# Kernel tuning notes

Measured on AMD Instinct MI355X. Metric: run time of the kernel, lower is better.

The kernel has to match this reference:

```python
import jax, jax.numpy as jnp
import numpy as np

B, D, E, K, HID, RH, NL, EMB = 4096, 1024, 8, 2, 512, 256, 24, 32


def _ln(y, g, b, eps=1e-5):
    mu = y.mean(-1, keepdims=True)
    var = y.var(-1, keepdims=True)
    return (y - mu) / jnp.sqrt(var + eps) * g + b


def setup_inputs() -> dict:
    key = jax.random.key(0)
    ks = jax.random.split(key, 16)
    s = 0.02
    return {
        "h": jax.random.normal(ks[0], (B, D), jnp.float32),
        "x": jax.random.normal(ks[1], (B, D), jnp.float32),
        "layer_idx": 5,
        "layer_emb": jax.random.normal(ks[2], (NL, EMB)) * s,
        "phase_emb": jax.random.normal(ks[3], (2, EMB)) * s,
        "Wr1": jax.random.normal(ks[4], (2 * D + 2 * EMB, RH)) * s,
        "br1": jnp.zeros((RH,)),
        "lnr_g": jnp.ones((RH,)),
        "lnr_b": jnp.zeros((RH,)),
        "Wr2": jax.random.normal(ks[5], (RH, E)) * s,
        "br2": jnp.zeros((E,)),
        "W1": jax.random.normal(ks[6], (E, 2 * D, HID)) * s,
        "b1": jnp.zeros((E, HID)),
        "ln1_g": jnp.ones((E, HID)),
        "ln1_b": jnp.zeros((E, HID)),
        "W2": jax.random.normal(ks[7], (E, HID, 4 * D)) * s,
        "b2": jnp.zeros((E, 4 * D)),
        "Wa": jax.random.normal(ks[8], (E, D, D)) * s,
        "ba": jnp.zeros((E, D)),
        "Wb": jax.random.normal(ks[9], (E, D, D)) * s,
        "bb": jnp.zeros((E, D)),
        "Wg": jax.random.normal(ks[10], (E, D, D)) * s,
        "bg": jnp.zeros((E, D)),
        "Wv": jax.random.normal(ks[11], (E, D, D)) * s,
        "bv": jnp.zeros((E, D)),
    }


def reference(h, x, layer_idx, layer_emb, phase_emb, Wr1, br1, lnr_g, lnr_b,
              Wr2, br2, W1, b1, ln1_g, ln1_b, W2, b2,
              Wa, ba, Wb, bb, Wg, bg, Wv, bv):
    Bn = h.shape[0]
    # --- router ---
    le = jnp.broadcast_to(layer_emb[layer_idx], (Bn, EMB))
    pe = jnp.broadcast_to(phase_emb[0], (Bn, EMB))  # phase='equilibrium' -> idx 0
    ri = jnp.concatenate([h, x, le, pe], axis=-1)   # [B, 2D+64]
    rhid = jax.nn.gelu(_ln(ri @ Wr1 + br1, lnr_g, lnr_b), approximate=False)
    logits = rhid @ Wr2 + br2                       # [B, E]
    top_vals, top_idx = jax.lax.top_k(logits, K)    # [B, K]
    w = jax.nn.softmax(top_vals, axis=-1)           # [B, K]
    # --- all experts (vectorized over E), then gather top-k per token ---
    hx = jnp.concatenate([h, x], axis=-1)           # [B, 2D]
    hid = jnp.einsum('bi,eio->ebo', hx, W1) + b1[:, None]          # [E, B, HID]
    hid = jax.nn.gelu(_ln(hid, ln1_g[:, None], ln1_b[:, None]), approximate=False)
    feats = jnp.einsum('ebh,eho->ebo', hid, W2) + b2[:, None]      # [E, B, 4D]
    af, bf, gf, vf = jnp.split(feats, 4, axis=-1)
    alpha = jax.nn.sigmoid(jnp.einsum('ebd,edo->ebo', af, Wa) + ba[:, None])
    beta = jax.nn.softplus(jnp.einsum('ebd,edo->ebo', bf, Wb) + bb[:, None])
    gate = jax.nn.sigmoid(jnp.einsum('ebd,edo->ebo', gf, Wg) + bg[:, None])
    vcd = jnp.einsum('ebd,edo->ebo', vf, Wv) + bv[:, None]
    allo = jnp.stack([alpha, beta, gate, vcd])       # [4, E, B, D]
    sel = allo[:, top_idx, jnp.arange(Bn)[:, None]]  # [4, B, K, D]
    out = jnp.einsum('bk,obkd->obd', w, sel)         # [4, B, D]
    return out
```

## Files before the change

kernel.cpp:

```cpp
#include <hip/hip_runtime.h>
#include <hip/hip_bf16.h>

#define B_TOK   4096
#define D_DIM   1024
#define E_NUM   8
#define HID_DIM 512
#define RH_DIM  256
#define EMB_DIM 32
#define NPAIR   (B_TOK * 2)
#define CPAD    32

typedef __attribute__((ext_vector_type(8))) short    bf16x8;
typedef __attribute__((ext_vector_type(8))) unsigned short u16x8;
typedef __attribute__((ext_vector_type(4))) unsigned short u16x4;
typedef __attribute__((ext_vector_type(4))) float    f32x4;

__device__ __forceinline__ unsigned short f2bf(float f) {
    union { float f; unsigned u; } v; v.f = f;
    unsigned r = (v.u + 0x7fffu + ((v.u >> 16) & 1u)) >> 16;
    return (unsigned short)r;
}
__device__ __forceinline__ float bf2f(unsigned short b) {
    union { unsigned u; float f; } v; v.u = ((unsigned)b) << 16;
    return v.f;
}

__device__ __forceinline__ void glds16(const void* g, void* l) {
    __builtin_amdgcn_global_load_lds(
        (const __attribute__((address_space(1))) unsigned int*)g,
        (__attribute__((address_space(3))) unsigned int*)l, 16, 0, 0);
}

__device__ inline float apply_act(float v, int a) {
    if (a == 0 || a == 2) return 1.f / (1.f + __expf(-v));
    if (a == 1) return fmaxf(v, 0.f) + __logf(1.f + __expf(-fabsf(v)));
    return v;
}

__global__ void k_hxbf(const float* __restrict__ h, const float* __restrict__ x,
                       unsigned short* __restrict__ hi, unsigned short* __restrict__ lo) {
    int gid = blockIdx.x * 256 + threadIdx.x;
    int token = gid >> 8;
    int c0 = (gid & 255) * 8;
    const float* src = (c0 < 1024) ? (h + (size_t)token * 1024 + c0)
                                   : (x + (size_t)token * 1024 + c0 - 1024);
    u16x8 oh, ol;
#pragma unroll
    for (int j = 0; j < 8; ++j) {
        float f = src[j];
        unsigned short hb = f2bf(f);
        oh[j] = hb;
        ol[j] = f2bf(f - bf2f(hb));
    }
    size_t o = (size_t)gid * 8;
    *(u16x8*)(hi + o) = oh;
    *(u16x8*)(lo + o) = ol;
}

__global__ void k_cvtflat(const float* __restrict__ in, unsigned short* __restrict__ o8) {
    size_t gid = (size_t)blockIdx.x * 256 + threadIdx.x;
    const float4* s = (const float4*)(in + gid * 8);
    float4 a = s[0], b = s[1];
    u16x8 v;
    v[0] = f2bf(a.x); v[1] = f2bf(a.y); v[2] = f2bf(a.z); v[3] = f2bf(a.w);
    v[4] = f2bf(b.x); v[5] = f2bf(b.y); v[6] = f2bf(b.z); v[7] = f2bf(b.w);
    *(u16x8*)(o8 + gid * 8) = v;
}

template<bool SPLIT>
__global__ void k_convW(const float* __restrict__ in0, const float* __restrict__ in1,
                        const float* __restrict__ in2, const float* __restrict__ in3,
                        unsigned short* __restrict__ oh, unsigned short* __restrict__ ol,
                        int K, int N, int eper) {
    int z = blockIdx.z;
    int e = z % eper, m = z / eper;
    const float* in = (m == 0 ? in0 : m == 1 ? in1 : m == 2 ? in2 : in3) + (size_t)e * K * N;
    int n  = blockIdx.x * 256 + threadIdx.x;
    int kg = blockIdx.y;
    const float* ip = in + (size_t)kg * 8 * N + n;
    u16x8 hv, lv;
#pragma unroll
    for (int j = 0; j < 8; ++j) {
        float f = ip[(size_t)j * N];
        unsigned short hb = f2bf(f);
        hv[j] = hb;
        if (SPLIT) lv[j] = f2bf(f - bf2f(hb));
    }
    size_t o = (size_t)z * K * N + ((size_t)kg * N + n) * 8;
    *(u16x8*)(oh + o) = hv;
    if (SPLIT) *(u16x8*)(ol + o) = lv;
}

__global__ void k_bfuse(const float* __restrict__ b2,
                        const float* __restrict__ bo0, const float* __restrict__ bo1,
                        const float* __restrict__ bo2, const float* __restrict__ bo3,
                        const unsigned short* __restrict__ wsc,
                        float* __restrict__ bfused) {
    int zp = blockIdx.y; int e = zp & 7, o = zp >> 3;
    int col = blockIdx.x * 256 + threadIdx.x;
    __shared__ float b2s[1024];
    for (int i = threadIdx.x; i < 1024; i += 256)
        b2s[i] = b2[(size_t)e * 4096 + o * 1024 + i];
    __syncthreads();
    const unsigned short* W = wsc + (size_t)zp * 1024 * 1024;
    float acc = 0.f;
    for (int dg = 0; dg < 128; ++dg) {
        u16x8 w = *(const u16x8*)&W[((size_t)dg * 1024 + col) * 8];
#pragma unroll
        for (int j = 0; j < 8; ++j) acc += b2s[dg * 8 + j] * bf2f(w[j]);
    }
    const float* bo = (o == 0) ? bo0 : (o == 1) ? bo1 : (o == 2) ? bo2 : bo3;
    bfused[(size_t)e * 4096 + o * 1024 + col] = acc + bo[(size_t)e * 1024 + col];
}

__global__ void k_route(const float* __restrict__ Pf,
                        const int* __restrict__ lidx,
                        const float* __restrict__ layer_emb,
                        const float* __restrict__ phase_emb,
                        const float* __restrict__ Wr1, const float* __restrict__ br1,
                        const float* __restrict__ lnr_g, const float* __restrict__ lnr_b,
                        const float* __restrict__ Wr2, const float* __restrict__ br2,
                        float* __restrict__ pair_w,
                        int* __restrict__ lists, int* __restrict__ counts) {
    int b = blockIdx.x, t = threadIdx.x;
    __shared__ float sv[RH_DIM];
    __shared__ float a1[4], a2[4], mv[2];
    __shared__ float wsum[4][E_NUM];
    __shared__ float lg[E_NUM];
    __shared__ int sei[2];

    float rc = br1[t];
    {
        int li = lidx[0];
        for (int k = 0; k < EMB_DIM; ++k)
            rc += layer_emb[li * EMB_DIM + k] * Wr1[(2048 + k) * RH_DIM + t];
        for (int k = 0; k < EMB_DIM; ++k)
            rc += phase_emb[k] * Wr1[(2080 + k) * RH_DIM + t];
    }

    size_t idx = (size_t)b * RH_DIM + t;
    const size_t kstride = (size_t)B_TOK * RH_DIM;
    float y = ((Pf[idx] + Pf[idx + kstride]) + (Pf[idx + 2 * kstride] + Pf[idx + 3 * kstride]))
              + rc;
    float s1 = y, s2 = y * y;
    for (int o = 32; o; o >>= 1) { s1 += __shfl_down(s1, o); s2 += __shfl_down(s2, o); }
    if ((t & 63) == 0) { a1[t >> 6] = s1; a2[t >> 6] = s2; }
    __syncthreads();
    if (t == 0) {
        float S1 = a1[0] + a1[1] + a1[2] + a1[3];
        float S2 = a2[0] + a2[1] + a2[2] + a2[3];
        float mu = S1 / 256.f;
        mv[0] = mu;
        mv[1] = rsqrtf(S2 / 256.f - mu * mu + 1e-5f);
    }
    __syncthreads();
    float n = (y - mv[0]) * mv[1] * lnr_g[t] + lnr_b[t];
    sv[t] = 0.5f * n * (1.f + erff(n * 0.70710678118654752f));
    __syncthreads();

    {
        int e = t & 7, c = t >> 3;
        float part = 0.f;
#pragma unroll
        for (int jj = 0; jj < 8; ++jj)
            part += sv[c * 8 + jj] * Wr2[(c * 8 + jj) * E_NUM + e];
        part += __shfl_down(part, 8);
        part += __shfl_down(part, 16);
        part += __shfl_down(part, 32);
        if ((t & 63) < 8) wsum[t >> 6][e] = part;
    }
    __syncthreads();
    if (t < E_NUM)
        lg[t] = br2[t] + wsum[0][t] + wsum[1][t] + wsum[2][t] + wsum[3][t];
    __syncthreads();
    if (t == 0) {
        float v0 = -1e30f; int i0 = 0;
        for (int e = 0; e < E_NUM; ++e) if (lg[e] > v0) { v0 = lg[e]; i0 = e; }
        float v1 = -1e30f; int i1 = 0;
        for (int e = 0; e < E_NUM; ++e) if (e != i0 && lg[e] > v1) { v1 = lg[e]; i1 = e; }
        float e1 = expf(v1 - v0);
        pair_w[2 * b] = 1.f / (1.f + e1);
        pair_w[2 * b + 1] = e1 / (1.f + e1);
        sei[0] = i0; sei[1] = i1;
    }
    __syncthreads();
    if (t < 2) {
        int e = sei[t];
        int pos = atomicAdd(&counts[e * CPAD], 1);
        lists[e * B_TOK + pos] = 2 * b + t;
    }
}

__global__ void k_meta(const int* __restrict__ counts, const int* __restrict__ lists,
                       int* __restrict__ rowmap, int* __restrict__ row_e,
                       int* __restrict__ qof) {
    int q = blockIdx.x * 256 + threadIdx.x;
    int off_[E_NUM + 1]; off_[0] = 0;
#pragma unroll
    for (int i = 0; i < E_NUM; ++i) off_[i + 1] = off_[i] + counts[i * CPAD];
    int e = 0;
    while (e < E_NUM - 1 && q >= off_[e + 1]) ++e;
    int p = lists[e * B_TOK + (q - off_[e])];
    rowmap[q] = p;
    row_e[q] = e;
    qof[p] = q;
}

__global__ void k_lngelu(const float* __restrict__ hidp, const float* __restrict__ b1,
                         unsigned short* __restrict__ hidb, const int* __restrict__ row_e,
                         const float* __restrict__ g, const float* __restrict__ bb) {
    int q = blockIdx.x, t = threadIdx.x;
    int e = row_e[q];
    const size_t st = (size_t)NPAIR * HID_DIM;
    size_t o0 = (size_t)q * HID_DIM + t;
    float y0 = hidp[o0] + hidp[o0 + st] + b1[e * HID_DIM + t];
    float y1 = hidp[o0 + 256] + hidp[o0 + 256 + st] + b1[e * HID_DIM + t + 256];
    float s1 = y0 + y1, s2 = y0 * y0 + y1 * y1;
    for (int o = 32; o; o >>= 1) { s1 += __shfl_down(s1, o); s2 += __shfl_down(s2, o); }
    __shared__ float a1[4], a2[4], mv[2];
    if ((t & 63) == 0) { a1[t >> 6] = s1; a2[t >> 6] = s2; }
    __syncthreads();
    if (t == 0) {
        float S1 = a1[0] + a1[1] + a1[2] + a1[3];
        float S2 = a2[0] + a2[1] + a2[2] + a2[3];
        float mu = S1 / 512.f;
        mv[0] = mu;
        mv[1] = rsqrtf(S2 / 512.f - mu * mu + 1e-5f);
    }
    __syncthreads();
    const float* ge = g + e * HID_DIM;
    const float* be = bb + e * HID_DIM;
    float mu = mv[0], ir = mv[1];
    float n0 = (y0 - mu) * ir * ge[t] + be[t];
    float n1 = (y1 - mu) * ir * ge[t + 256] + be[t + 256];
    unsigned short* orow = hidb + (size_t)q * HID_DIM;
    orow[t]       = f2bf(0.5f * n0 * (1.f + erff(n0 * 0.70710678118654752f)));
    orow[t + 256] = f2bf(0.5f * n1 * (1.f + erff(n1 * 0.70710678118654752f)));
}

__global__ void k_comb(const unsigned short* __restrict__ sel,
                       const int* __restrict__ qof, const float* __restrict__ pw,
                       float* __restrict__ out) {
    int b = blockIdx.x, o = blockIdx.y;
    int c = threadIdx.x * 4;
    int q0 = qof[2 * b], q1 = qof[2 * b + 1];
    float w0 = pw[2 * b], w1 = pw[2 * b + 1];
    u16x4 a = __builtin_nontemporal_load((const u16x4*)(sel + (size_t)q0 * 4096 + o * 1024 + c));
    u16x4 bq = __builtin_nontemporal_load((const u16x4*)(sel + (size_t)q1 * 4096 + o * 1024 + c));
    f32x4 r;
#pragma unroll
    for (int j = 0; j < 4; ++j)
        r[j] = w0 * apply_act(bf2f(a[j]), o) + w1 * apply_act(bf2f(bq[j]), o);
    __builtin_nontemporal_store(r, (f32x4*)(out + ((size_t)o * B_TOK + b) * D_DIM + c));
}

template<int MODE, bool SPLIT, bool AGATHER, bool ZPIN>
__global__ __launch_bounds__(256)
void k_mm(const unsigned short* __restrict__ A, const unsigned short* __restrict__ Alo,
          int lda, int rowshift, int acol0,
          const unsigned short* __restrict__ Wp, const unsigned short* __restrict__ Wlo,
          size_t wstride,
          const float* __restrict__ bias, int bstride,
          float* __restrict__ Cf, unsigned short* __restrict__ Cb, int ldc,
          const int* __restrict__ counts, const int* __restrict__ rowmap, int Mfix,
          int N, int Nfull, int Kdim, int nz_e,
          float* __restrict__ outp, const float* __restrict__ pw) {
    const int gx = gridDim.x, gy = gridDim.y;
    unsigned fb = blockIdx.x + gx * (blockIdx.y + gy * blockIdx.z);
    int bx, byy, bz;
    if (ZPIN) {
        const unsigned nmn = gx * gy;
        unsigned xcd = fb & 7u, s = fb >> 3;
        bz  = xcd + 8u * (s / nmn);
        unsigned inner = s % nmn;
        bx  = inner % gx;
        byy = inner / gx;
    } else {
        unsigned xcd = fb & 7u, sb = fb >> 3;
        unsigned G = xcd + 8u * (sb / gx);
        bx  = sb % gx;
        byy = G % gy;
        bz  = G / gy;
    }

    const int e  = bz % nz_e;
    const int zq = bz / nz_e;
    int cnt = Mfix, base = 0;
    if (counts) {
        cnt = 0;
#pragma unroll
        for (int i = 0; i < E_NUM; ++i) {
            int c = counts[i * CPAD];
            if (i < e) base += c;
            if (i == e) cnt = c;
        }
    }
    const int n0 = bx * 128;

    const size_t woff = (MODE == 8) ? (size_t)bz * wstride
                      : (MODE == 1 || MODE == 9) ? (size_t)e * wstride
                      : (size_t)e * wstride + (size_t)zq * Kdim * N;
    const unsigned short* W  = Wp + woff;
    const unsigned short* Wl = SPLIT ? (Wlo + woff) : nullptr;
    const float* bptr = (MODE == 1 || MODE == 9) ? bias + (size_t)e * bstride : nullptr;
    const int acol = acol0 + ((MODE == 4 || MODE == 5 || MODE == 8) ? zq * Kdim : 0);
    const int ncb  = (MODE == 1) ? zq * N : 0;

    constexpr int ABUF = SPLIT ? 8192 : 4096;
    __shared__ unsigned short Alds[2][ABUF];
    __shared__ unsigned short Blds[2][ABUF];

    const int tid  = threadIdx.x;
    const int lane = tid & 63;
    const int wid  = tid >> 6;
    const int c0 = tid, c1 = tid + 256;
    const int r0 = c0 >> 2, r1 = c1 >> 2;

    const int wm = wid >> 1, wn = wid & 1;
    const int lr = lane & 15, lg = lane >> 4;
    const int aslot = (lg ^ ((lr >> 1) & 3)) << 3;
    const int d0 = c0 * 8, d1 = c1 * 8;
    const size_t bstep = (size_t)32 * Nfull;

    for (int mt = byy; mt * 128 < cnt; mt += gy) {
        const int m0 = mt * 128;

        auto aoff_of = [&](int r, int cq) -> size_t {
            int rr = m0 + r; if (rr >= cnt) rr = cnt - 1;
            int qg = base + rr;
            int row = AGATHER ? (rowmap[qg] >> rowshift)
                              : (MODE == 8 ? e * 512 + qg : qg);
            int slot = cq ^ ((r >> 1) & 3);
            return (size_t)row * lda + acol + (slot << 3);
        };
        size_t aoff0 = aoff_of(r0, c0 & 3);
        size_t aoff1 = aoff_of(r1, c1 & 3);
        const unsigned short* a0 = A + aoff0;
        const unsigned short* a1 = A + aoff1;
        const unsigned short* al0 = SPLIT ? Alo + aoff0 : nullptr;
        const unsigned short* al1 = SPLIT ? Alo + aoff1 : nullptr;
        size_t boff0 = ((size_t)(c0 >> 7) * Nfull + ncb + n0 + (c0 & 127)) * 8;
        size_t boff1 = ((size_t)(c1 >> 7) * Nfull + ncb + n0 + (c1 & 127)) * 8;
        const unsigned short* b0 = W + boff0;
        const unsigned short* b1 = W + boff1;
        const unsigned short* bl0 = SPLIT ? Wl + boff0 : nullptr;
        const unsigned short* bl1 = SPLIT ? Wl + boff1 : nullptr;

        auto stage = [&](int buf) {
            glds16(a0, &Alds[buf][d0]);
            glds16(a1, &Alds[buf][d1]);
            glds16(b0, &Blds[buf][d0]);
            glds16(b1, &Blds[buf][d1]);
            if constexpr (SPLIT) {
                glds16(al0, &Alds[buf][4096 + d0]);
                glds16(al1, &Alds[buf][4096 + d1]);
                glds16(bl0, &Blds[buf][4096 + d0]);
                glds16(bl1, &Blds[buf][4096 + d1]);
                al0 += 32; al1 += 32; bl0 += bstep; bl1 += bstep;
            }
            a0 += 32; a1 += 32; b0 += bstep; b1 += bstep;
        };

        f32x4 acc[4][4];
#pragma unroll
        for (int i = 0; i < 4; ++i)
#pragma unroll
            for (int j = 0; j < 4; ++j) acc[i][j] = (f32x4){0.f, 0.f, 0.f, 0.f};

        auto compute = [&](int b) {
            bf16x8 af[4], bfr[4];
#pragma unroll
            for (int i = 0; i < 4; ++i)
                af[i] = *(const bf16x8*)&Alds[b][(wm * 64 + i * 16 + lr) * 32 + aslot];
#pragma unroll
            for (int i = 0; i < 4; ++i)
                bfr[i] = *(const bf16x8*)&Blds[b][((lg << 7) + wn * 64 + i * 16 + lr) * 8];
            __builtin_amdgcn_s_setprio(1);
#pragma unroll
            for (int mi = 0; mi < 4; ++mi)
#pragma unroll
                for (int ni = 0; ni < 4; ++ni)
                    acc[mi][ni] = __builtin_amdgcn_mfma_f32_16x16x32_bf16(af[mi], bfr[ni], acc[mi][ni], 0, 0, 0);
            if constexpr (SPLIT) {
                bf16x8 afl[4], bfl[4];
#pragma unroll
                for (int i = 0; i < 4; ++i)
                    afl[i] = *(const bf16x8*)&Alds[b][4096 + (wm * 64 + i * 16 + lr) * 32 + aslot];
#pragma unroll
                for (int i = 0; i < 4; ++i)
                    bfl[i] = *(const bf16x8*)&Blds[b][4096 + ((lg << 7) + wn * 64 + i * 16 + lr) * 8];
#pragma unroll
                for (int mi = 0; mi < 4; ++mi)
#pragma unroll
                    for (int ni = 0; ni < 4; ++ni) {
                        acc[mi][ni] = __builtin_amdgcn_mfma_f32_16x16x32_bf16(af[mi],  bfl[ni], acc[mi][ni], 0, 0, 0);
                        acc[mi][ni] = __builtin_amdgcn_mfma_f32_16x16x32_bf16(afl[mi], bfr[ni], acc[mi][ni], 0, 0, 0);
                    }
            }
            __builtin_amdgcn_s_setprio(0);
            __builtin_amdgcn_sched_barrier(0);
        };

        const int niter = Kdim / 32;
        stage(0);
        asm volatile("s_waitcnt vmcnt(0)" ::: "memory");
        __builtin_amdgcn_s_barrier();
        __builtin_amdgcn_sched_barrier(0);
        int cur = 0;
        for (int it = 0; it < niter; ++it) {
            const bool more = (it + 1 < niter);
            if (more) stage(cur ^ 1);
            compute(cur);
            if (more) {
                asm volatile("s_waitcnt vmcnt(0)" ::: "memory");
                __builtin_amdgcn_s_barrier();
                __builtin_amdgcn_sched_barrier(0);
            }
            cur ^= 1;
        }
        __builtin_amdgcn_s_barrier();

        float bv[4];
#pragma unroll
        for (int ni = 0; ni < 4; ++ni)
            bv[ni] = (MODE == 1 || MODE == 9) ? bptr[ncb + n0 + wn * 64 + ni * 16 + lr] : 0.f;

#pragma unroll
        for (int mi = 0; mi < 4; ++mi) {
            int rbase = m0 + wm * 64 + mi * 16 + lg * 4;
#pragma unroll
            for (int rg = 0; rg < 4; ++rg) {
                int r = rbase + rg;
                if (r >= cnt) continue;
                int q = base + r;
#pragma unroll
                for (int ni = 0; ni < 4; ++ni) {
                    int col = ncb + n0 + wn * 64 + ni * 16 + lr;
                    float v = acc[mi][ni][rg] + bv[ni];
                    if (MODE == 1) {
                        Cb[(size_t)q * ldc + col] = f2bf(v);
                    } else if (MODE == 4) {
                        Cf[((size_t)zq * B_TOK + q) * ldc + col] = v;
                    } else if (MODE == 5) {
                        Cf[((size_t)zq * NPAIR + q) * ldc + col] = v;
                    } else if (MODE == 8) {
                        Cb[((size_t)e * 64 * 4096 + (size_t)(r >> 3) * 4096 + acol + col) * 8
                           + (r & 7)] = f2bf(v);
                    } else {
                        int p = rowmap[q];
                        int o = col >> 10;
                        atomicAdd(outp + ((size_t)o * B_TOK + (p >> 1)) * D_DIM + (col & 1023),
                                  pw[p] * apply_act(v, o));
                    }
                }
            }
        }
    }
}

extern "C" void kernel_launch(void* const* d_in, const int* in_sizes, int n_in,
                              void* d_out, int out_size, void* d_ws, size_t ws_size,
                              hipStream_t stream) {
    const float* h         = (const float*)d_in[0];
    const float* x         = (const float*)d_in[1];
    const int*   lidx      = (const int*)d_in[2];
    const float* layer_emb = (const float*)d_in[3];
    const float* phase_emb = (const float*)d_in[4];
    const float* Wr1       = (const float*)d_in[5];
    const float* br1       = (const float*)d_in[6];
    const float* lnr_g     = (const float*)d_in[7];
    const float* lnr_b     = (const float*)d_in[8];
    const float* Wr2       = (const float*)d_in[9];
    const float* br2       = (const float*)d_in[10];
    const float* W1        = (const float*)d_in[11];
    const float* b1        = (const float*)d_in[12];
    const float* ln1g      = (const float*)d_in[13];
    const float* ln1b      = (const float*)d_in[14];
    const float* W2        = (const float*)d_in[15];
    const float* b2        = (const float*)d_in[16];
    const float* Wa        = (const float*)d_in[17];
    const float* ba        = (const float*)d_in[18];
    const float* Wb_       = (const float*)d_in[19];
    const float* bbv       = (const float*)d_in[20];
    const float* Wg        = (const float*)d_in[21];
    const float* bg        = (const float*)d_in[22];
    const float* Wv        = (const float*)d_in[23];
    const float* bv        = (const float*)d_in[24];
    float* out = (float*)d_out;

    char* ws = (char*)d_ws;
    size_t off = 0;
    auto alloc = [&](size_t nb) { void* p = ws + off; off = (off + nb + 255) & ~(size_t)255; return p; };
    float*          pair_w  = (float*)alloc(NPAIR * 4);
    int*            counts  = (int*)alloc(E_NUM * CPAD * 4);
    int*            lists   = (int*)alloc((size_t)E_NUM * B_TOK * 4);
    int*            rowmap  = (int*)alloc(NPAIR * 4);
    int*            row_e   = (int*)alloc(NPAIR * 4);
    int*            qof     = (int*)alloc(NPAIR * 4);
    float*          bfused  = (float*)alloc((size_t)E_NUM * 4096 * 4);
    unsigned short* hx_hi   = (unsigned short*)alloc((size_t)B_TOK * 2048 * 2);
    unsigned short* hid_bf  = (unsigned short*)alloc((size_t)NPAIR * HID_DIM * 2);
    unsigned short* wsc_hi  = (unsigned short*)alloc((size_t)8 * 2048 * HID_DIM * 2);
    unsigned short* wsc_lo  = (unsigned short*)alloc((size_t)2048 * RH_DIM * 2);
    unsigned short* Wfused  = (unsigned short*)alloc((size_t)E_NUM * 64 * 4096 * 8 * 2);
    unsigned short* sel     = (unsigned short*)alloc((size_t)NPAIR * 4096 * 2);
    char*           scratch = (char*)alloc((size_t)34 << 20);
    const bool use_sel = (off <= ws_size);
    unsigned short* wsc4  = sel;
    unsigned short* W2bf  = (unsigned short*)scratch;
    unsigned short* hx_lo = (unsigned short*)scratch;
    float*          Pf    = (float*)(scratch + ((size_t)17 << 20));
    float*          hidp  = (float*)scratch;

    if (!use_sel) (void)hipMemsetAsync(d_out, 0, (size_t)out_size * 4, stream);
    (void)hipMemsetAsync(counts, 0, E_NUM * CPAD * 4, stream);

    k_hxbf<<<4096, 256, 0, stream>>>(h, x, hx_hi, hx_lo);
    k_convW<true><<<dim3(1, 256, 1), 256, 0, stream>>>(Wr1, nullptr, nullptr, nullptr,
                                                       wsc_hi, wsc_lo, 2048, RH_DIM, 1);
    k_mm<4, true, false, false><<<dim3(2, 32, 4), 256, 0, stream>>>(
        hx_hi, hx_lo, 2048, 0, 0, wsc_hi, wsc_lo, 0, nullptr, 0,
        Pf, nullptr, RH_DIM, nullptr, nullptr, B_TOK,
        RH_DIM, RH_DIM, 512, 1, nullptr, nullptr);
    k_route<<<B_TOK, 256, 0, stream>>>(Pf, lidx, layer_emb, phase_emb, Wr1, br1,
                                       lnr_g, lnr_b, Wr2, br2,
                                       pair_w, lists, counts);
    k_meta<<<NPAIR / 256, 256, 0, stream>>>(counts, lists, rowmap, row_e, qof);

    k_convW<false><<<dim3(2, 256, 8), 256, 0, stream>>>(W1, nullptr, nullptr, nullptr,
                                                        wsc_hi, nullptr, 2048, HID_DIM, 8);
    k_mm<5, false, true, true><<<dim3(4, 9, 16), 256, 0, stream>>>(
        hx_hi, nullptr, 2048, 1, 0, wsc_hi, nullptr, (size_t)2048 * HID_DIM, nullptr, 0,
        hidp, nullptr, HID_DIM, counts, rowmap, 0,
        HID_DIM, HID_DIM, 1024, 8, nullptr, nullptr);
    k_lngelu<<<NPAIR, 256, 0, stream>>>(hidp, b1, hid_bf, row_e, ln1g, ln1b);

    k_cvtflat<<<8192, 256, 0, stream>>>(W2, W2bf);
    k_convW<false><<<dim3(4, 128, 32), 256, 0, stream>>>(
        Wa, Wb_, Wg, Wv, wsc4, nullptr, D_DIM, D_DIM, 8);
    k_bfuse<<<dim3(4, 32), 256, 0, stream>>>(b2, ba, bbv, bg, bv, wsc4, bfused);
    k_mm<8, false, false, true><<<dim3(8, 4, 32), 256, 0, stream>>>(
        W2bf, nullptr, 4096, 0, 0,
        wsc4, nullptr, (size_t)D_DIM * D_DIM, nullptr, 0,
        nullptr, Wfused, 0, nullptr, nullptr, 512,
        D_DIM, D_DIM, D_DIM, 8, nullptr, nullptr);

    if (use_sel) {
        k_mm<1, false, false, true><<<dim3(16, 9, 16), 256, 0, stream>>>(
            hid_bf, nullptr, HID_DIM, 0, 0,
            Wfused, nullptr, (size_t)64 * 4096 * 8, bfused, 4096,
            nullptr, sel, 4096, counts, rowmap, 0,
            2048, 4096, HID_DIM, 8, nullptr, nullptr);
        k_comb<<<dim3(B_TOK, 4), 256, 0, stream>>>(sel, qof, pair_w, out);
    } else {
        k_mm<9, false, false, true><<<dim3(32, 32, 8), 256, 0, stream>>>(
            hid_bf, nullptr, HID_DIM, 0, 0,
            Wfused, nullptr, (size_t)64 * 4096 * 8, bfused, 4096,
            nullptr, nullptr, 0, counts, rowmap, 0,
            4096, 4096, HID_DIM, 8, out, pair_w);
    }
}
```

Measured before the change: 422.4 us.

## Launch one block per M tile in grouped GEMMs and hoist router constant

The grouped expert GEMM kernel now handles one 128-row M tile per block with an early exit, replacing the loop that strode over tiles by gridDim.y. The expert GEMM grids grow from 9 to 32 in y so any expert count up to 4096 rows is covered. This removes load imbalance from skewed expert counts, at the cost of launching many blocks that exit immediately. Separately, the router's layer/phase embedding projection is computed once in a small kernel instead of once per token block.

```diff
diff --git a/kernel.cpp b/kernel.cpp
--- a/kernel.cpp
+++ b/kernel.cpp
@@ -113,11 +113,23 @@
     bfused[(size_t)e * 4096 + o * 1024 + col] = acc + bo[(size_t)e * 1024 + col];
 }
 
-__global__ void k_route(const float* __restrict__ Pf,
-                        const int* __restrict__ lidx,
-                        const float* __restrict__ layer_emb,
-                        const float* __restrict__ phase_emb,
-                        const float* __restrict__ Wr1, const float* __restrict__ br1,
+__global__ void k_rconst(const float* __restrict__ layer_emb,
+                         const float* __restrict__ phase_emb,
+                         const int* __restrict__ lidx,
+                         const float* __restrict__ Wr1,
+                         const float* __restrict__ br1,
+                         float* __restrict__ rconst) {
+    int j = threadIdx.x;
+    int li = lidx[0];
+    float acc = br1[j];
+    for (int t = 0; t < EMB_DIM; ++t)
+        acc += layer_emb[li * EMB_DIM + t] * Wr1[(2048 + t) * RH_DIM + j];
+    for (int t = 0; t < EMB_DIM; ++t)
+        acc += phase_emb[t] * Wr1[(2080 + t) * RH_DIM + j];
+    rconst[j] = acc;
+}
+
+__global__ void k_route(const float* __restrict__ Pf, const float* __restrict__ rconst,
                         const float* __restrict__ lnr_g, const float* __restrict__ lnr_b,
                         const float* __restrict__ Wr2, const float* __restrict__ br2,
                         float* __restrict__ pair_w,
@@ -129,19 +141,10 @@
     __shared__ float lg[E_NUM];
     __shared__ int sei[2];
 
-    float rc = br1[t];
-    {
-        int li = lidx[0];
-        for (int k = 0; k < EMB_DIM; ++k)
-            rc += layer_emb[li * EMB_DIM + k] * Wr1[(2048 + k) * RH_DIM + t];
-        for (int k = 0; k < EMB_DIM; ++k)
-            rc += phase_emb[k] * Wr1[(2080 + k) * RH_DIM + t];
-    }
-
     size_t idx = (size_t)b * RH_DIM + t;
     const size_t kstride = (size_t)B_TOK * RH_DIM;
     float y = ((Pf[idx] + Pf[idx + kstride]) + (Pf[idx + 2 * kstride] + Pf[idx + 3 * kstride]))
-              + rc;
+              + rconst[t];
     float s1 = y, s2 = y * y;
     for (int o = 32; o; o >>= 1) { s1 += __shfl_down(s1, o); s2 += __shfl_down(s2, o); }
     if ((t & 63) == 0) { a1[t >> 6] = s1; a2[t >> 6] = s2; }
@@ -295,6 +298,8 @@
             if (i == e) cnt = c;
         }
     }
+    const int m0 = byy * 128;
+    if (m0 >= cnt) return;
     const int n0 = bx * 128;
 
     const size_t woff = (MODE == 8) ? (size_t)bz * wstride
@@ -316,142 +321,138 @@
     const int c0 = tid, c1 = tid + 256;
     const int r0 = c0 >> 2, r1 = c1 >> 2;
 
+    auto aoff_of = [&](int r, int cq) -> size_t {
+        int rr = m0 + r; if (rr >= cnt) rr = cnt - 1;
+        int qg = base + rr;
+        int row = AGATHER ? (rowmap[qg] >> rowshift)
+                          : (MODE == 8 ? e * 512 + qg : qg);
+        int slot = cq ^ ((r >> 1) & 3);
+        return (size_t)row * lda + acol + (slot << 3);
+    };
+    size_t aoff0 = aoff_of(r0, c0 & 3);
+    size_t aoff1 = aoff_of(r1, c1 & 3);
+    const unsigned short* a0 = A + aoff0;
+    const unsigned short* a1 = A + aoff1;
+    const unsigned short* al0 = SPLIT ? Alo + aoff0 : nullptr;
+    const unsigned short* al1 = SPLIT ? Alo + aoff1 : nullptr;
+    size_t boff0 = ((size_t)(c0 >> 7) * Nfull + ncb + n0 + (c0 & 127)) * 8;
+    size_t boff1 = ((size_t)(c1 >> 7) * Nfull + ncb + n0 + (c1 & 127)) * 8;
+    const unsigned short* b0 = W + boff0;
+    const unsigned short* b1 = W + boff1;
+    const unsigned short* bl0 = SPLIT ? Wl + boff0 : nullptr;
+    const unsigned short* bl1 = SPLIT ? Wl + boff1 : nullptr;
+
+    const int d0 = c0 * 8, d1 = c1 * 8;
+    const size_t bstep = (size_t)32 * Nfull;
+
+    auto stage = [&](int buf) {
+        glds16(a0, &Alds[buf][d0]);
+        glds16(a1, &Alds[buf][d1]);
+        glds16(b0, &Blds[buf][d0]);
+        glds16(b1, &Blds[buf][d1]);
+        if constexpr (SPLIT) {
+            glds16(al0, &Alds[buf][4096 + d0]);
+            glds16(al1, &Alds[buf][4096 + d1]);
+            glds16(bl0, &Blds[buf][4096 + d0]);
+            glds16(bl1, &Blds[buf][4096 + d1]);
+            al0 += 32; al1 += 32; bl0 += bstep; bl1 += bstep;
+        }
+        a0 += 32; a1 += 32; b0 += bstep; b1 += bstep;
+    };
+
     const int wm = wid >> 1, wn = wid & 1;
     const int lr = lane & 15, lg = lane >> 4;
     const int aslot = (lg ^ ((lr >> 1) & 3)) << 3;
-    const int d0 = c0 * 8, d1 = c1 * 8;
-    const size_t bstep = (size_t)32 * Nfull;
-
-    for (int mt = byy; mt * 128 < cnt; mt += gy) {
-        const int m0 = mt * 128;
-
-        auto aoff_of = [&](int r, int cq) -> size_t {
-            int rr = m0 + r; if (rr >= cnt) rr = cnt - 1;
-            int qg = base + rr;
-            int row = AGATHER ? (rowmap[qg] >> rowshift)
-                              : (MODE == 8 ? e * 512 + qg : qg);
-            int slot = cq ^ ((r >> 1) & 3);
-            return (size_t)row * lda + acol + (slot << 3);
-        };
-        size_t aoff0 = aoff_of(r0, c0 & 3);
-        size_t aoff1 = aoff_of(r1, c1 & 3);
-        const unsigned short* a0 = A + aoff0;
-        const unsigned short* a1 = A + aoff1;
-        const unsigned short* al0 = SPLIT ? Alo + aoff0 : nullptr;
-        const unsigned short* al1 = SPLIT ? Alo + aoff1 : nullptr;
-        size_t boff0 = ((size_t)(c0 >> 7) * Nfull + ncb + n0 + (c0 & 127)) * 8;
-        size_t boff1 = ((size_t)(c1 >> 7) * Nfull + ncb + n0 + (c1 & 127)) * 8;
-        const unsigned short* b0 = W + boff0;
-        const unsigned short* b1 = W + boff1;
-        const unsigned short* bl0 = SPLIT ? Wl + boff0 : nullptr;
-        const unsigned short* bl1 = SPLIT ? Wl + boff1 : nullptr;
-
-        auto stage = [&](int buf) {
-            glds16(a0, &Alds[buf][d0]);
-            glds16(a1, &Alds[buf][d1]);
-            glds16(b0, &Blds[buf][d0]);
-            glds16(b1, &Blds[buf][d1]);
-            if constexpr (SPLIT) {
-                glds16(al0, &Alds[buf][4096 + d0]);
-                glds16(al1, &Alds[buf][4096 + d1]);
-                glds16(bl0, &Blds[buf][4096 + d0]);
-                glds16(bl1, &Blds[buf][4096 + d1]);
-                al0 += 32; al1 += 32; bl0 += bstep; bl1 += bstep;
-            }
-            a0 += 32; a1 += 32; b0 += bstep; b1 += bstep;
-        };
-
-        f32x4 acc[4][4];
+
+    f32x4 acc[4][4];
+#pragma unroll
+    for (int i = 0; i < 4; ++i)
+#pragma unroll
+        for (int j = 0; j < 4; ++j) acc[i][j] = (f32x4){0.f, 0.f, 0.f, 0.f};
+
+    auto compute = [&](int b) {
+        bf16x8 af[4], bfr[4];
 #pragma unroll
         for (int i = 0; i < 4; ++i)
-#pragma unroll
-            for (int j = 0; j < 4; ++j) acc[i][j] = (f32x4){0.f, 0.f, 0.f, 0.f};
-
-        auto compute = [&](int b) {
-            bf16x8 af[4], bfr[4];
+            af[i] = *(const bf16x8*)&Alds[b][(wm * 64 + i * 16 + lr) * 32 + aslot];
+#pragma unroll
+        for (int i = 0; i < 4; ++i)
+            bfr[i] = *(const bf16x8*)&Blds[b][((lg << 7) + wn * 64 + i * 16 + lr) * 8];
+        __builtin_amdgcn_s_setprio(1);
+#pragma unroll
+        for (int mi = 0; mi < 4; ++mi)
+#pragma unroll
+            for (int ni = 0; ni < 4; ++ni)
+                acc[mi][ni] = __builtin_amdgcn_mfma_f32_16x16x32_bf16(af[mi], bfr[ni], acc[mi][ni], 0, 0, 0);
+        if constexpr (SPLIT) {
+            bf16x8 afl[4], bfl[4];
 #pragma unroll
             for (int i = 0; i < 4; ++i)
-                af[i] = *(const bf16x8*)&Alds[b][(wm * 64 + i * 16 + lr) * 32 + aslot];
+                afl[i] = *(const bf16x8*)&Alds[b][4096 + (wm * 64 + i * 16 + lr) * 32 + aslot];
 #pragma unroll
             for (int i = 0; i < 4; ++i)
-                bfr[i] = *(const bf16x8*)&Blds[b][((lg << 7) + wn * 64 + i * 16 + lr) * 8];
-            __builtin_amdgcn_s_setprio(1);
+                bfl[i] = *(const bf16x8*)&Blds[b][4096 + ((lg << 7) + wn * 64 + i * 16 + lr) * 8];
 #pragma unroll
             for (int mi = 0; mi < 4; ++mi)
 #pragma unroll
-                for (int ni = 0; ni < 4; ++ni)
-                    acc[mi][ni] = __builtin_amdgcn_mfma_f32_16x16x32_bf16(af[mi], bfr[ni], acc[mi][ni], 0, 0, 0);
-            if constexpr (SPLIT) {
-                bf16x8 afl[4], bfl[4];
-#pragma unroll
-                for (int i = 0; i < 4; ++i)
-                    afl[i] = *(const bf16x8*)&Alds[b][4096 + (wm * 64 + i * 16 + lr) * 32 + aslot];
-#pragma unroll
-                for (int i = 0; i < 4; ++i)
-                    bfl[i] = *(const bf16x8*)&Blds[b][4096 + ((lg << 7) + wn * 64 + i * 16 + lr) * 8];
-#pragma unroll
-                for (int mi = 0; mi < 4; ++mi)
-#pragma unroll
-                    for (int ni = 0; ni < 4; ++ni) {
-                        acc[mi][ni] = __builtin_amdgcn_mfma_f32_16x16x32_bf16(af[mi],  bfl[ni], acc[mi][ni], 0, 0, 0);
-                        acc[mi][ni] = __builtin_amdgcn_mfma_f32_16x16x32_bf16(afl[mi], bfr[ni], acc[mi][ni], 0, 0, 0);
-                    }
-            }
-            __builtin_amdgcn_s_setprio(0);
+                for (int ni = 0; ni < 4; ++ni) {
+                    acc[mi][ni] = __builtin_amdgcn_mfma_f32_16x16x32_bf16(af[mi],  bfl[ni], acc[mi][ni], 0, 0, 0);
+                    acc[mi][ni] = __builtin_amdgcn_mfma_f32_16x16x32_bf16(afl[mi], bfr[ni], acc[mi][ni], 0, 0, 0);
+                }
+        }
+        __builtin_amdgcn_s_setprio(0);
+        __builtin_amdgcn_sched_barrier(0);
+    };
+
+    const int niter = Kdim / 32;
+    stage(0);
+    asm volatile("s_waitcnt vmcnt(0)" ::: "memory");
+    __builtin_amdgcn_s_barrier();
+    __builtin_amdgcn_sched_barrier(0);
+    int cur = 0;
+    for (int it = 0; it < niter; ++it) {
+        const bool more = (it + 1 < niter);
+        if (more) stage(cur ^ 1);
+        compute(cur);
+        if (more) {
+            asm volatile("s_waitcnt vmcnt(0)" ::: "memory");
+            __builtin_amdgcn_s_barrier();
             __builtin_amdgcn_sched_barrier(0);
-        };
-
-        const int niter = Kdim / 32;
-        stage(0);
-        asm volatile("s_waitcnt vmcnt(0)" ::: "memory");
-        __builtin_amdgcn_s_barrier();
-        __builtin_amdgcn_sched_barrier(0);
-        int cur = 0;
-        for (int it = 0; it < niter; ++it) {
-            const bool more = (it + 1 < niter);
-            if (more) stage(cur ^ 1);
-            compute(cur);
-            if (more) {
-                asm volatile("s_waitcnt vmcnt(0)" ::: "memory");
-                __builtin_amdgcn_s_barrier();
-                __builtin_amdgcn_sched_barrier(0);
-            }
-            cur ^= 1;
         }
-        __builtin_amdgcn_s_barrier();
-
-        float bv[4];
-#pragma unroll
-        for (int ni = 0; ni < 4; ++ni)
-            bv[ni] = (MODE == 1 || MODE == 9) ? bptr[ncb + n0 + wn * 64 + ni * 16 + lr] : 0.f;
-
-#pragma unroll
-        for (int mi = 0; mi < 4; ++mi) {
-            int rbase = m0 + wm * 64 + mi * 16 + lg * 4;
-#pragma unroll
-            for (int rg = 0; rg < 4; ++rg) {
-                int r = rbase + rg;
-                if (r >= cnt) continue;
-                int q = base + r;
-#pragma unroll
-                for (int ni = 0; ni < 4; ++ni) {
-                    int col = ncb + n0 + wn * 64 + ni * 16 + lr;
-                    float v = acc[mi][ni][rg] + bv[ni];
-                    if (MODE == 1) {
-                        Cb[(size_t)q * ldc + col] = f2bf(v);
-                    } else if (MODE == 4) {
-                        Cf[((size_t)zq * B_TOK + q) * ldc + col] = v;
-                    } else if (MODE == 5) {
-                        Cf[((size_t)zq * NPAIR + q) * ldc + col] = v;
-                    } else if (MODE == 8) {
-                        Cb[((size_t)e * 64 * 4096 + (size_t)(r >> 3) * 4096 + acol + col) * 8
-                           + (r & 7)] = f2bf(v);
-                    } else {
-                        int p = rowmap[q];
-                        int o = col >> 10;
-                        atomicAdd(outp + ((size_t)o * B_TOK + (p >> 1)) * D_DIM + (col & 1023),
-                                  pw[p] * apply_act(v, o));
-                    }
+        cur ^= 1;
+    }
+
+    float bv[4];
+#pragma unroll
+    for (int ni = 0; ni < 4; ++ni)
+        bv[ni] = (MODE == 1 || MODE == 9) ? bptr[ncb + n0 + wn * 64 + ni * 16 + lr] : 0.f;
+
+#pragma unroll
+    for (int mi = 0; mi < 4; ++mi) {
+        int rbase = m0 + wm * 64 + mi * 16 + lg * 4;
+#pragma unroll
+        for (int rg = 0; rg < 4; ++rg) {
+            int r = rbase + rg;
+            if (r >= cnt) continue;
+            int q = base + r;
+#pragma unroll
+            for (int ni = 0; ni < 4; ++ni) {
+                int col = ncb + n0 + wn * 64 + ni * 16 + lr;
+                float v = acc[mi][ni][rg] + bv[ni];
+                if (MODE == 1) {
+                    Cb[(size_t)q * ldc + col] = f2bf(v);
+                } else if (MODE == 4) {
+                    Cf[((size_t)zq * B_TOK + q) * ldc + col] = v;
+                } else if (MODE == 5) {
+                    Cf[((size_t)zq * NPAIR + q) * ldc + col] = v;
+                } else if (MODE == 8) {
+                    Cb[((size_t)e * 64 * 4096 + (size_t)(r >> 3) * 4096 + acol + col) * 8
+                       + (r & 7)] = f2bf(v);
+                } else {
+                    int p = rowmap[q];
+                    int o = col >> 10;
+                    atomicAdd(outp + ((size_t)o * B_TOK + (p >> 1)) * D_DIM + (col & 1023),
+                              pw[p] * apply_act(v, o));
                 }
             }
         }
@@ -491,6 +492,7 @@
     char* ws = (char*)d_ws;
     size_t off = 0;
     auto alloc = [&](size_t nb) { void* p = ws + off; off = (off + nb + 255) & ~(size_t)255; return p; };
+    float*          rconstp = (float*)alloc(RH_DIM * 4);
     float*          pair_w  = (float*)alloc(NPAIR * 4);
     int*            counts  = (int*)alloc(E_NUM * CPAD * 4);
     int*            lists   = (int*)alloc((size_t)E_NUM * B_TOK * 4);
@@ -518,18 +520,18 @@
     k_hxbf<<<4096, 256, 0, stream>>>(h, x, hx_hi, hx_lo);
     k_convW<true><<<dim3(1, 256, 1), 256, 0, stream>>>(Wr1, nullptr, nullptr, nullptr,
                                                        wsc_hi, wsc_lo, 2048, RH_DIM, 1);
+    k_rconst<<<1, 256, 0, stream>>>(layer_emb, phase_emb, lidx, Wr1, br1, rconstp);
     k_mm<4, true, false, false><<<dim3(2, 32, 4), 256, 0, stream>>>(
         hx_hi, hx_lo, 2048, 0, 0, wsc_hi, wsc_lo, 0, nullptr, 0,
         Pf, nullptr, RH_DIM, nullptr, nullptr, B_TOK,
         RH_DIM, RH_DIM, 512, 1, nullptr, nullptr);
-    k_route<<<B_TOK, 256, 0, stream>>>(Pf, lidx, layer_emb, phase_emb, Wr1, br1,
-                                       lnr_g, lnr_b, Wr2, br2,
+    k_route<<<B_TOK, 256, 0, stream>>>(Pf, rconstp, lnr_g, lnr_b, Wr2, br2,
                                        pair_w, lists, counts);
     k_meta<<<NPAIR / 256, 256, 0, stream>>>(counts, lists, rowmap, row_e, qof);
 
     k_convW<false><<<dim3(2, 256, 8), 256, 0, stream>>>(W1, nullptr, nullptr, nullptr,
                                                         wsc_hi, nullptr, 2048, HID_DIM, 8);
-    k_mm<5, false, true, true><<<dim3(4, 9, 16), 256, 0, stream>>>(
+    k_mm<5, false, true, true><<<dim3(4, 32, 16), 256, 0, stream>>>(
         hx_hi, nullptr, 2048, 1, 0, wsc_hi, nullptr, (size_t)2048 * HID_DIM, nullptr, 0,
         hidp, nullptr, HID_DIM, counts, rowmap, 0,
         HID_DIM, HID_DIM, 1024, 8, nullptr, nullptr);
@@ -546,7 +548,7 @@
         D_DIM, D_DIM, D_DIM, 8, nullptr, nullptr);
 
     if (use_sel) {
-        k_mm<1, false, false, true><<<dim3(16, 9, 16), 256, 0, stream>>>(
+        k_mm<1, false, false, true><<<dim3(16, 32, 16), 256, 0, stream>>>(
             hid_bf, nullptr, HID_DIM, 0, 0,
             Wfused, nullptr, (size_t)64 * 4096 * 8, bfused, 4096,
             nullptr, sel, 4096, counts, rowmap, 0,
```

Measured after the change: 399.0 us (median of 2 runs). 1.06x faster.
